# Performance work log

Hardware: AMD Instinct MI355X
Metric: run time of the kernel (lower is better)

Reference implementation:

```python
import jax, jax.numpy as jnp
import numpy as np

TEMPERATURE = 0.07
HARD_NEG_WEIGHT = 0.5
MARGIN = 0.2
NUM_HARD_NEG = 3
BATCH = 8192
DIM = 256
NUM_CLASSES = 512


def setup_inputs() -> dict:
    key = jax.random.key(0)
    k1, k2 = jax.random.split(key)
    embeddings = jax.random.normal(k1, (BATCH, DIM), dtype=jnp.float32)
    labels = jax.random.randint(k2, (BATCH,), 0, NUM_CLASSES, dtype=jnp.int64)
    return {"embeddings": embeddings, "labels": labels}


def reference(embeddings, labels):
    B = embeddings.shape[0]
    dt = embeddings.dtype
    # L2 normalize (torch F.normalize with eps clamp)
    norm = jnp.maximum(jnp.linalg.norm(embeddings, axis=-1, keepdims=True), 1e-12)
    e = embeddings / norm
    sim = jnp.matmul(e, e.T) / TEMPERATURE  # [B, B]

    same = (labels[:, None] == labels[None, :]).astype(dt)
    eye = jnp.eye(B, dtype=dt)
    pos_mask = same - eye            # positives excluding self
    neg_mask = 1.0 - same            # negatives (diag is 0 since labels==labels)

    # basic InfoNCE-style loss (unnormalized exp, as in the original)
    exp_sim = jnp.exp(sim) * (1.0 - eye)
    pos_sim = (exp_sim * pos_mask).sum(axis=-1)
    all_sim = exp_sim.sum(axis=-1)
    basic = -jnp.log(pos_sim / (all_sim + 1e-10) + 1e-10)
    has_pos = pos_mask.sum(axis=-1) > 0
    hp = has_pos.astype(dt)
    n_hp = jnp.maximum(hp.sum(), 1.0)
    basic_loss = (basic * hp).sum() / n_hp

    # hard negative mining: top-k most similar negatives vs best positive
    neg_inf = -jnp.inf
    neg_sim = jnp.where(neg_mask > 0, sim, neg_inf)
    k = min(NUM_HARD_NEG, B - 1)
    hard_neg_mean = jax.lax.top_k(neg_sim, k)[0].mean(axis=-1)
    pos_max = jnp.where(pos_mask > 0, sim, neg_inf).max(axis=-1)
    h = jax.nn.relu(hard_neg_mean - pos_max + MARGIN)
    h = jnp.where(has_pos, h, 0.0)
    hard_loss = (h * hp).sum() / n_hp

    # margin ranking: max positive vs max negative
    max_neg = neg_sim.max(axis=-1)
    m = jax.nn.relu(max_neg - pos_max + MARGIN)
    valid = (pos_max > neg_inf) & (max_neg > neg_inf)
    v = valid.astype(dt)
    n_v = jnp.maximum(v.sum(), 1.0)
    margin_loss = jnp.where(v.sum() > 0, jnp.where(valid, m, 0.0).sum() / n_v, 0.0)

    total = basic_loss + HARD_NEG_WEIGHT * hard_loss + 0.1 * margin_loss
    return total
```

## Files before the change

kernel.cpp:

```cpp
#include <hip/hip_runtime.h>
#include <cstdint>
#include <cstddef>

#define BATCH  8192
#define DIM    256
#define NSTRIP 16
#define SCOLS  512
#define MROWS  128
#define NTILE  64
#define NITER  (SCOLS/NTILE)

static constexpr float INV_T   = 1.0f / 0.07f;
static constexpr float EXP2_SC = 1.4426950408889634f / 0.07f;
static constexpr float MARGIN  = 0.2f;

typedef __attribute__((ext_vector_type(8))) short short8;
typedef __attribute__((ext_vector_type(4))) float f32x4;

__device__ __forceinline__ unsigned short f2bf(float f){
  unsigned int u = __float_as_uint(f);
  u += 0x7FFFu + ((u >> 16) & 1u);
  return (unsigned short)(u >> 16);
}

__device__ __forceinline__ void ins3(float& t0, float& t1, float& t2, float s){
  float m0 = fmaxf(t0, s); float r1 = fminf(t0, s); t0 = m0;
  float m1 = fmaxf(t1, r1); float r2 = fminf(t1, r1); t1 = m1;
  t2 = fmaxf(t2, r2);
}

__global__ void norm_cast_kernel(const float* __restrict__ emb,
                                 unsigned short* __restrict__ E,
                                 float* __restrict__ accum){
  if (blockIdx.x == 0 && threadIdx.x < 8) accum[threadIdx.x] = 0.0f;
  const int wave = threadIdx.x >> 6;
  const int lane = threadIdx.x & 63;
  const int row  = blockIdx.x * 4 + wave;
  const float4 v = *(const float4*)(emb + (size_t)row * DIM + lane * 4);
  float ss = v.x*v.x + v.y*v.y + v.z*v.z + v.w*v.w;
  #pragma unroll
  for (int m = 1; m < 64; m <<= 1) ss += __shfl_xor(ss, m, 64);
  float nrm = fmaxf(sqrtf(ss), 1e-12f);
  float inv = 1.0f / nrm;
  ushort4 o;
  o.x = f2bf(v.x * inv); o.y = f2bf(v.y * inv);
  o.z = f2bf(v.z * inv); o.w = f2bf(v.w * inv);
  *(ushort4*)(E + (size_t)row * DIM + lane * 4) = o;
}

__global__ __launch_bounds__(256, 2)
void sim_stats_kernel(const unsigned short* __restrict__ E,
                      const int* __restrict__ labels,
                      float* __restrict__ partials){
  const int strip = blockIdx.x;
  const int rb    = blockIdx.y * MROWS;
  const int cs    = strip * SCOLS;
  const int tid   = threadIdx.x;
  const int wave  = tid >> 6;
  const int lane  = tid & 63;
  const int l     = lane & 15;
  const int q     = lane >> 4;

  __shared__ short8 Bs[32 * 64];
  __shared__ int labs[SCOLS];

  for (int i = tid; i < SCOLS; i += 256) labs[i] = labels[cs + i];

  const int row0 = rb + wave * 32;

  short8 a[2][8];
  #pragma unroll
  for (int rt = 0; rt < 2; ++rt){
    const unsigned short* rp = E + (size_t)(row0 + rt*16 + l) * DIM + q * 8;
    #pragma unroll
    for (int kk = 0; kk < 8; ++kk)
      a[rt][kk] = *(const short8*)(rp + kk * 32);
  }

  int labr[2][4];
  #pragma unroll
  for (int rt = 0; rt < 2; ++rt)
    #pragma unroll
    for (int rr = 0; rr < 4; ++rr)
      labr[rt][rr] = labels[row0 + rt*16 + q*4 + rr];

  float all_s[8], pos_s[8], pos_m[8], t0[8], t1[8], t2[8];
  #pragma unroll
  for (int s = 0; s < 8; ++s){
    all_s[s] = 0.f; pos_s[s] = 0.f;
    pos_m[s] = -INFINITY; t0[s] = -INFINITY; t1[s] = -INFINITY; t2[s] = -INFINITY;
  }

  for (int it = 0; it < NITER; ++it){
    const int cb = cs + it * NTILE;
    __syncthreads();
    #pragma unroll
    for (int ci = 0; ci < 8; ++ci){
      const int c = wave * 8 + ci;
      const unsigned short* g = E + (size_t)(cb + lane) * DIM + c * 8;
      __builtin_amdgcn_global_load_lds(
        (const __attribute__((address_space(1))) unsigned int*)g,
        (__attribute__((address_space(3))) unsigned int*)&Bs[c * 64],
        16, 0, 0);
    }
    __syncthreads();

    #pragma unroll
    for (int t = 0; t < 4; ++t){
      const int gcol = cb + t * 16 + l;
      const int labc = labs[it * NTILE + t * 16 + l];
      f32x4 acc0 = {0.f,0.f,0.f,0.f};
      f32x4 acc1 = {0.f,0.f,0.f,0.f};
      #pragma unroll
      for (int kk = 0; kk < 8; ++kk){
        short8 b = Bs[(kk * 4 + q) * 64 + t * 16 + l];
        acc0 = __builtin_amdgcn_mfma_f32_16x16x32_bf16(a[0][kk], b, acc0, 0, 0, 0);
        acc1 = __builtin_amdgcn_mfma_f32_16x16x32_bf16(a[1][kk], b, acc1, 0, 0, 0);
      }
      #pragma unroll
      for (int rt = 0; rt < 2; ++rt){
        #pragma unroll
        for (int rr = 0; rr < 4; ++rr){
          const float d    = rt ? acc1[rr] : acc0[rr];
          const int   s    = rt * 4 + rr;
          const int   grow = row0 + rt * 16 + q * 4 + rr;
          const float ex   = __builtin_amdgcn_exp2f(d * EXP2_SC);
          const bool same  = (labc == labr[rt][rr]);
          const bool self  = (gcol == grow);
          all_s[s] += self ? 0.f : ex;
          const bool ispos = same && !self;
          pos_s[s] += ispos ? ex : 0.f;
          pos_m[s]  = fmaxf(pos_m[s], ispos ? d : -INFINITY);
          const float sn = same ? -INFINITY : d;
          ins3(t0[s], t1[s], t2[s], sn);
        }
      }
    }
  }

  #pragma unroll
  for (int mask = 1; mask < 16; mask <<= 1){
    #pragma unroll
    for (int s = 0; s < 8; ++s){
      all_s[s] += __shfl_xor(all_s[s], mask, 64);
      pos_s[s] += __shfl_xor(pos_s[s], mask, 64);
      pos_m[s]  = fmaxf(pos_m[s], __shfl_xor(pos_m[s], mask, 64));
      float b0 = __shfl_xor(t0[s], mask, 64);
      float b1 = __shfl_xor(t1[s], mask, 64);
      float b2 = __shfl_xor(t2[s], mask, 64);
      ins3(t0[s], t1[s], t2[s], b0);
      ins3(t0[s], t1[s], t2[s], b1);
      ins3(t0[s], t1[s], t2[s], b2);
    }
  }

  if (l == 0){
    #pragma unroll
    for (int s = 0; s < 8; ++s){
      const int grow = row0 + (s >> 2) * 16 + q * 4 + (s & 3);
      float* p = partials + (size_t)(strip * 6) * BATCH + grow;
      p[0]                   = all_s[s];
      p[(size_t)BATCH]       = pos_s[s];
      p[(size_t)2 * BATCH]   = pos_m[s];
      p[(size_t)3 * BATCH]   = t0[s];
      p[(size_t)4 * BATCH]   = t1[s];
      p[(size_t)5 * BATCH]   = t2[s];
    }
  }
}

__global__ void merge_kernel(const float* __restrict__ partials,
                             float* __restrict__ accum){
  const int row = blockIdx.x * 256 + threadIdx.x;
  float all_s = 0.f, pos_s = 0.f, pos_m = -INFINITY;
  float t0 = -INFINITY, t1 = -INFINITY, t2 = -INFINITY;
  #pragma unroll
  for (int s = 0; s < NSTRIP; ++s){
    const float* p = partials + (size_t)(s * 6) * BATCH + row;
    all_s += p[0];
    pos_s += p[(size_t)BATCH];
    pos_m  = fmaxf(pos_m, p[(size_t)2 * BATCH]);
    ins3(t0, t1, t2, p[(size_t)3 * BATCH]);
    ins3(t0, t1, t2, p[(size_t)4 * BATCH]);
    ins3(t0, t1, t2, p[(size_t)5 * BATCH]);
  }
  pos_m *= INV_T; t0 *= INV_T; t1 *= INV_T; t2 *= INV_T;

  const bool has_pos = pos_m > -INFINITY;
  float vb = 0.f, vh = 0.f, vhp = 0.f, vm = 0.f, vv = 0.f;
  if (has_pos){
    vhp = 1.f;
    vb  = -logf(pos_s / (all_s + 1e-10f) + 1e-10f);
    const float hnm = (t0 + t1 + t2) * (1.f/3.f);
    vh  = fmaxf(hnm - pos_m + MARGIN, 0.f);
    if (t0 > -INFINITY){
      vv = 1.f;
      vm = fmaxf(t0 - pos_m + MARGIN, 0.f);
    }
  }
  float vals[5] = {vb, vh, vhp, vm, vv};
  #pragma unroll
  for (int m = 1; m < 64; m <<= 1)
    #pragma unroll
    for (int i = 0; i < 5; ++i) vals[i] += __shfl_xor(vals[i], m, 64);
  if ((threadIdx.x & 63) == 0){
    #pragma unroll
    for (int i = 0; i < 5; ++i) atomicAdd(&accum[i], vals[i]);
  }
}

__global__ void final_kernel(const float* __restrict__ accum,
                             float* __restrict__ out){
  if (threadIdx.x == 0){
    const float nhp   = fmaxf(accum[2], 1.f);
    const float basic = accum[0] / nhp;
    const float hard  = accum[1] / nhp;
    const float marg  = (accum[4] > 0.f) ? (accum[3] / fmaxf(accum[4], 1.f)) : 0.f;
    out[0] = basic + 0.5f * hard + 0.1f * marg;
  }
}

extern "C" void kernel_launch(void* const* d_in, const int* in_sizes, int n_in,
                              void* d_out, int out_size, void* d_ws, size_t ws_size,
                              hipStream_t stream){
  const float* emb  = (const float*)d_in[0];
  const int* labels = (const int*)d_in[1];
  float* out        = (float*)d_out;
  char* ws          = (char*)d_ws;

  unsigned short* E = (unsigned short*)ws;
  const size_t E_BYTES = (size_t)BATCH * DIM * 2;
  float* partials   = (float*)(ws + E_BYTES);
  const size_t P_BYTES = (size_t)NSTRIP * 6 * BATCH * sizeof(float);
  float* accum      = (float*)(ws + E_BYTES + P_BYTES);

  norm_cast_kernel<<<BATCH/4, 256, 0, stream>>>(emb, E, accum);
  sim_stats_kernel<<<dim3(NSTRIP, BATCH/MROWS), 256, 0, stream>>>(E, labels, partials);
  merge_kernel<<<BATCH/256, 256, 0, stream>>>(partials, accum);
  final_kernel<<<1, 64, 0, stream>>>(accum, out);
}
```

Before: 156.0 us.

## Compute positive-pair stats via label buckets instead of in the dense epilogue

Groups row indices into per-label buckets and computes positive sum and max with a separate sparse kernel that only touches same-label pairs. This removes pos_s and pos_m tracking and the self-mask test from the hot MFMA epilogue, handling the diagonal with a subtraction only on diagonal tiles. It also uses fmed3 in the top-3 insertion, shrinks the partials from 6 to 4 arrays, and raises launch bounds to 3 waves per SIMD. It adds two extra kernel launches and caps buckets at 96 entries, which could silently drop positives if a label has more samples than that.

```diff
diff --git a/kernel.cpp b/kernel.cpp
--- a/kernel.cpp
+++ b/kernel.cpp
@@ -9,6 +9,7 @@
 #define MROWS  128
 #define NTILE  64
 #define NITER  (SCOLS/NTILE)
+#define BCAP   96
 
 static constexpr float INV_T   = 1.0f / 0.07f;
 static constexpr float EXP2_SC = 1.4426950408889634f / 0.07f;
@@ -24,15 +25,19 @@
 }
 
 __device__ __forceinline__ void ins3(float& t0, float& t1, float& t2, float s){
-  float m0 = fmaxf(t0, s); float r1 = fminf(t0, s); t0 = m0;
-  float m1 = fmaxf(t1, r1); float r2 = fminf(t1, r1); t1 = m1;
-  t2 = fmaxf(t2, r2);
+  float m0  = fmaxf(t0, s);
+  float mid = __builtin_amdgcn_fmed3f(t0, t1, s);
+  float lo  = fminf(fminf(t0, t1), s);
+  t2 = fmaxf(t2, lo);
+  t0 = m0; t1 = mid;
 }
 
 __global__ void norm_cast_kernel(const float* __restrict__ emb,
                                  unsigned short* __restrict__ E,
-                                 float* __restrict__ accum){
+                                 float* __restrict__ accum,
+                                 int* __restrict__ bcnt){
   if (blockIdx.x == 0 && threadIdx.x < 8) accum[threadIdx.x] = 0.0f;
+  if (blockIdx.x < 2) bcnt[blockIdx.x * 256 + threadIdx.x] = 0;
   const int wave = threadIdx.x >> 6;
   const int lane = threadIdx.x & 63;
   const int row  = blockIdx.x * 4 + wave;
@@ -48,7 +53,49 @@
   *(ushort4*)(E + (size_t)row * DIM + lane * 4) = o;
 }
 
-__global__ __launch_bounds__(256, 2)
+__global__ void bucket_build_kernel(const int* __restrict__ labels,
+                                    int* __restrict__ bcnt,
+                                    int* __restrict__ bucket){
+  const int i = blockIdx.x * 256 + threadIdx.x;
+  const int lab = labels[i];
+  const int idx = atomicAdd(&bcnt[lab], 1);
+  if (idx < BCAP) bucket[lab * BCAP + idx] = i;
+}
+
+__global__ void positives_kernel(const unsigned short* __restrict__ E,
+                                 const int* __restrict__ labels,
+                                 const int* __restrict__ bcnt,
+                                 const int* __restrict__ bucket,
+                                 float* __restrict__ posS,
+                                 float* __restrict__ posM){
+  const int wave = threadIdx.x >> 6;
+  const int lane = threadIdx.x & 63;
+  const int row  = blockIdx.x * 4 + wave;
+  const int lab  = labels[row];
+  const int n    = min(bcnt[lab], BCAP);
+  const unsigned short* ei = E + (size_t)row * DIM + lane * 4;
+  float a0 = __uint_as_float((unsigned)ei[0] << 16);
+  float a1 = __uint_as_float((unsigned)ei[1] << 16);
+  float a2 = __uint_as_float((unsigned)ei[2] << 16);
+  float a3 = __uint_as_float((unsigned)ei[3] << 16);
+  float ps = 0.f, pm = -INFINITY;
+  for (int j = 0; j < n; ++j){
+    const int col = bucket[lab * BCAP + j];
+    if (col == row) continue;
+    const unsigned short* ec = E + (size_t)col * DIM + lane * 4;
+    float d = a0 * __uint_as_float((unsigned)ec[0] << 16);
+    d = fmaf(a1, __uint_as_float((unsigned)ec[1] << 16), d);
+    d = fmaf(a2, __uint_as_float((unsigned)ec[2] << 16), d);
+    d = fmaf(a3, __uint_as_float((unsigned)ec[3] << 16), d);
+    #pragma unroll
+    for (int m = 1; m < 64; m <<= 1) d += __shfl_xor(d, m, 64);
+    ps += __builtin_amdgcn_exp2f(d * EXP2_SC);
+    pm = fmaxf(pm, d);
+  }
+  if (lane == 0){ posS[row] = ps; posM[row] = pm; }
+}
+
+__global__ __launch_bounds__(256, 3)
 void sim_stats_kernel(const unsigned short* __restrict__ E,
                       const int* __restrict__ labels,
                       float* __restrict__ partials){
@@ -84,11 +131,10 @@
     for (int rr = 0; rr < 4; ++rr)
       labr[rt][rr] = labels[row0 + rt*16 + q*4 + rr];
 
-  float all_s[8], pos_s[8], pos_m[8], t0[8], t1[8], t2[8];
+  float all_s[8], t0[8], t1[8], t2[8];
   #pragma unroll
   for (int s = 0; s < 8; ++s){
-    all_s[s] = 0.f; pos_s[s] = 0.f;
-    pos_m[s] = -INFINITY; t0[s] = -INFINITY; t1[s] = -INFINITY; t2[s] = -INFINITY;
+    all_s[s] = 0.f; t0[s] = -INFINITY; t1[s] = -INFINITY; t2[s] = -INFINITY;
   }
 
   for (int it = 0; it < NITER; ++it){
@@ -107,7 +153,6 @@
 
     #pragma unroll
     for (int t = 0; t < 4; ++t){
-      const int gcol = cb + t * 16 + l;
       const int labc = labs[it * NTILE + t * 16 + l];
       f32x4 acc0 = {0.f,0.f,0.f,0.f};
       f32x4 acc1 = {0.f,0.f,0.f,0.f};
@@ -121,19 +166,22 @@
       for (int rt = 0; rt < 2; ++rt){
         #pragma unroll
         for (int rr = 0; rr < 4; ++rr){
-          const float d    = rt ? acc1[rr] : acc0[rr];
-          const int   s    = rt * 4 + rr;
-          const int   grow = row0 + rt * 16 + q * 4 + rr;
-          const float ex   = __builtin_amdgcn_exp2f(d * EXP2_SC);
-          const bool same  = (labc == labr[rt][rr]);
-          const bool self  = (gcol == grow);
-          all_s[s] += self ? 0.f : ex;
-          const bool ispos = same && !self;
-          pos_s[s] += ispos ? ex : 0.f;
-          pos_m[s]  = fmaxf(pos_m[s], ispos ? d : -INFINITY);
-          const float sn = same ? -INFINITY : d;
+          const float d  = rt ? acc1[rr] : acc0[rr];
+          const int   s  = rt * 4 + rr;
+          const float ex = __builtin_amdgcn_exp2f(d * EXP2_SC);
+          all_s[s] += ex;
+          const bool same = (labc == labr[rt][rr]);
+          const float sn  = same ? -INFINITY : d;
           ins3(t0[s], t1[s], t2[s], sn);
         }
+        if (cb + t * 16 == row0 + rt * 16){
+          #pragma unroll
+          for (int rr = 0; rr < 4; ++rr){
+            const float d = rt ? acc1[rr] : acc0[rr];
+            const int   s = rt * 4 + rr;
+            all_s[s] -= (l == q * 4 + rr) ? __builtin_amdgcn_exp2f(d * EXP2_SC) : 0.f;
+          }
+        }
       }
     }
   }
@@ -143,8 +191,6 @@
     #pragma unroll
     for (int s = 0; s < 8; ++s){
       all_s[s] += __shfl_xor(all_s[s], mask, 64);
-      pos_s[s] += __shfl_xor(pos_s[s], mask, 64);
-      pos_m[s]  = fmaxf(pos_m[s], __shfl_xor(pos_m[s], mask, 64));
       float b0 = __shfl_xor(t0[s], mask, 64);
       float b1 = __shfl_xor(t1[s], mask, 64);
       float b2 = __shfl_xor(t2[s], mask, 64);
@@ -158,32 +204,32 @@
     #pragma unroll
     for (int s = 0; s < 8; ++s){
       const int grow = row0 + (s >> 2) * 16 + q * 4 + (s & 3);
-      float* p = partials + (size_t)(strip * 6) * BATCH + grow;
-      p[0]                   = all_s[s];
-      p[(size_t)BATCH]       = pos_s[s];
-      p[(size_t)2 * BATCH]   = pos_m[s];
-      p[(size_t)3 * BATCH]   = t0[s];
-      p[(size_t)4 * BATCH]   = t1[s];
-      p[(size_t)5 * BATCH]   = t2[s];
+      float* p = partials + (size_t)(strip * 4) * BATCH + grow;
+      p[0]                 = all_s[s];
+      p[(size_t)BATCH]     = t0[s];
+      p[(size_t)2 * BATCH] = t1[s];
+      p[(size_t)3 * BATCH] = t2[s];
     }
   }
 }
 
 __global__ void merge_kernel(const float* __restrict__ partials,
+                             const float* __restrict__ posS,
+                             const float* __restrict__ posM,
                              float* __restrict__ accum){
   const int row = blockIdx.x * 256 + threadIdx.x;
-  float all_s = 0.f, pos_s = 0.f, pos_m = -INFINITY;
+  float all_s = 0.f;
   float t0 = -INFINITY, t1 = -INFINITY, t2 = -INFINITY;
   #pragma unroll
   for (int s = 0; s < NSTRIP; ++s){
-    const float* p = partials + (size_t)(s * 6) * BATCH + row;
+    const float* p = partials + (size_t)(s * 4) * BATCH + row;
     all_s += p[0];
-    pos_s += p[(size_t)BATCH];
-    pos_m  = fmaxf(pos_m, p[(size_t)2 * BATCH]);
+    ins3(t0, t1, t2, p[(size_t)BATCH]);
+    ins3(t0, t1, t2, p[(size_t)2 * BATCH]);
     ins3(t0, t1, t2, p[(size_t)3 * BATCH]);
-    ins3(t0, t1, t2, p[(size_t)4 * BATCH]);
-    ins3(t0, t1, t2, p[(size_t)5 * BATCH]);
-  }
+  }
+  const float pos_s = posS[row];
+  float pos_m = posM[row];
   pos_m *= INV_T; t0 *= INV_T; t1 *= INV_T; t2 *= INV_T;
 
   const bool has_pos = pos_m > -INFINITY;
@@ -228,14 +274,19 @@
   float* out        = (float*)d_out;
   char* ws          = (char*)d_ws;
 
-  unsigned short* E = (unsigned short*)ws;
-  const size_t E_BYTES = (size_t)BATCH * DIM * 2;
-  float* partials   = (float*)(ws + E_BYTES);
-  const size_t P_BYTES = (size_t)NSTRIP * 6 * BATCH * sizeof(float);
-  float* accum      = (float*)(ws + E_BYTES + P_BYTES);
-
-  norm_cast_kernel<<<BATCH/4, 256, 0, stream>>>(emb, E, accum);
+  size_t off = 0;
+  unsigned short* E = (unsigned short*)(ws + off); off += (size_t)BATCH * DIM * 2;
+  float* partials   = (float*)(ws + off);          off += (size_t)NSTRIP * 4 * BATCH * 4;
+  float* posS       = (float*)(ws + off);          off += (size_t)BATCH * 4;
+  float* posM       = (float*)(ws + off);          off += (size_t)BATCH * 4;
+  int*   bcnt       = (int*)(ws + off);            off += 512 * 4;
+  int*   bucket     = (int*)(ws + off);            off += (size_t)512 * BCAP * 4;
+  float* accum      = (float*)(ws + off);          off += 8 * 4;
+
+  norm_cast_kernel<<<BATCH/4, 256, 0, stream>>>(emb, E, accum, bcnt);
+  bucket_build_kernel<<<BATCH/256, 256, 0, stream>>>(labels, bcnt, bucket);
+  positives_kernel<<<BATCH/4, 256, 0, stream>>>(E, labels, bcnt, bucket, posS, posM);
   sim_stats_kernel<<<dim3(NSTRIP, BATCH/MROWS), 256, 0, stream>>>(E, labels, partials);
-  merge_kernel<<<BATCH/256, 256, 0, stream>>>(partials, accum);
+  merge_kernel<<<BATCH/256, 256, 0, stream>>>(partials, posS, posM, accum);
   final_kernel<<<1, 64, 0, stream>>>(accum, out);
 }
```

New measurement: 177.6 us. +13.9%, slower.
